# Optimization experiments

Hardware: AMD Instinct MI355X
Metric: run time of the kernel (lower is better)

## Reference

```python
import jax, jax.numpy as jnp
import numpy as np

V_IPC, N_ROLES, D = 50000, 16, 256
B, L = 2048, 64
F_BIB, H1, H2, D_OUT = 512, 1024, 1024, 512
N_EXP, N_CLS = 8, 10
LN_EPS = 1e-5


def setup_inputs() -> dict:
    key = jax.random.key(0)
    ks = jax.random.split(key, 24)
    s = 0.05
    ipc_emb = jax.random.normal(ks[0], (V_IPC, D), jnp.float32) * s
    ipc_emb = ipc_emb.at[0].set(0.0)  # padding_idx=0
    role_emb = jax.random.normal(ks[1], (N_ROLES, D), jnp.float32) * s
    role_emb = role_emb.at[0].set(0.0)
    inp = {
        "ipc_indices": jax.random.randint(ks[2], (B, L), 0, V_IPC),
        "role_indices": jax.random.randint(ks[3], (B, L), 0, N_ROLES),
        "bibliometric_features": jax.random.normal(ks[4], (B, F_BIB), jnp.float32),
        "ipc_padding_mask": jax.random.randint(ks[5], (B, L), 0, 2).astype(jnp.int32),
        "top_k": 2,
        "ipc_emb": ipc_emb,
        "role_emb": role_emb,
        "Wq": jax.random.normal(ks[6], (D, D), jnp.float32) * s,
        "bq": jnp.zeros((D,), jnp.float32),
        "Wk": jax.random.normal(ks[7], (D, D), jnp.float32) * s,
        "bk": jnp.zeros((D,), jnp.float32),
        "Wv": jax.random.normal(ks[8], (D, D), jnp.float32) * s,
        "bv": jnp.zeros((D,), jnp.float32),
        "global_context": jax.random.normal(ks[9], (D,), jnp.float32) * s,
        "ln_g": jnp.ones((D,), jnp.float32),
        "ln_b": jnp.zeros((D,), jnp.float32),
        "gate_W": jax.random.normal(ks[10], (D, N_EXP), jnp.float32) * s,
        "gate_b": jnp.zeros((N_EXP,), jnp.float32),
        "expert_biases": jnp.zeros((N_EXP,), jnp.float32),
        "W1": jax.random.normal(ks[11], (N_EXP, F_BIB, H1), jnp.float32) * s,
        "b1": jnp.zeros((N_EXP, H1), jnp.float32),
        "W2": jax.random.normal(ks[12], (N_EXP, H1, H2), jnp.float32) * s,
        "b2": jnp.zeros((N_EXP, H2), jnp.float32),
        "W3": jax.random.normal(ks[13], (N_EXP, H2, D_OUT), jnp.float32) * s,
        "b3": jnp.zeros((N_EXP, D_OUT), jnp.float32),
        "head_W": jax.random.normal(ks[14], (D_OUT, N_CLS), jnp.float32) * s,
        "head_b": jnp.zeros((N_CLS,), jnp.float32),
    }
    return inp


def reference(ipc_indices, role_indices, bibliometric_features, ipc_padding_mask, top_k,
              ipc_emb, role_emb, Wq, bq, Wk, bk, Wv, bv, global_context, ln_g, ln_b,
              gate_W, gate_b, expert_biases, W1, b1, W2, b2, W3, b3, head_W, head_b):
    # embeddings + role combine  -> [B, L, D]
    x = ipc_emb[ipc_indices] + role_emb[role_indices]
    # attention pooling with a global learned query (same query for every batch row)
    keys = x @ Wk + bk                                  # [B, L, D]
    values = x @ Wv + bv                                # [B, L, D]
    q = global_context @ Wq + bq                        # [D]
    scores = jnp.einsum('d,bld->bl', q, keys)           # [B, L]
    scores = jnp.where(ipc_padding_mask == 0, -1e9, scores)
    attn = jax.nn.softmax(scores, axis=-1)              # [B, L]
    pooled = jnp.einsum('bl,bld->bd', attn, values)     # [B, D]
    mu = pooled.mean(-1, keepdims=True)
    var = ((pooled - mu) ** 2).mean(-1, keepdims=True)
    router_in = (pooled - mu) / jnp.sqrt(var + LN_EPS) * ln_g + ln_b
    # router: select with biased scores, gate with unbiased scores
    affinity = router_in @ gate_W + gate_b              # [B, E]
    sel_scores = affinity + expert_biases
    _, idx = jax.lax.top_k(sel_scores, top_k)           # [B, K]
    gw = jax.nn.softmax(jnp.take_along_axis(affinity, idx, axis=-1), axis=-1)  # [B, K]
    # dense all-expert MLP (reference form of masked per-expert loop)
    h = jax.nn.relu(jnp.einsum('bi,eih->ebh', bibliometric_features, W1) + b1[:, None, :])
    h = jax.nn.relu(jnp.einsum('ebh,ehj->ebj', h, W2) + b2[:, None, :])
    eo = jnp.einsum('ebj,ejo->ebo', h, W3) + b3[:, None, :]  # [E, B, O]
    # gather each token's top-k expert outputs and combine
    bidx = jnp.arange(idx.shape[0])[:, None]            # [B, 1]
    sel_out = eo[idx, bidx]                             # [B, K, O]
    moe_out = jnp.einsum('bk,bko->bo', gw, sel_out)     # [B, O]
    logits = moe_out @ head_W + head_b                  # [B, n_classes]
    return logits, idx
```

## Files before the change

### kernel.cpp

```cpp
#include <hip/hip_runtime.h>
#include <hip/hip_bf16.h>
#include <math.h>


#define LN_EPS 1e-5f

typedef __bf16 bf16_t;
typedef __bf16 bf16x8 __attribute__((ext_vector_type(8)));
typedef float f32x4 __attribute__((ext_vector_type(4)));

struct f4x2 { float4 a, b; };
__device__ __forceinline__ f4x2 ldA8(const float* p) {
  f4x2 v; v.a = *(const float4*)p; v.b = *(const float4*)(p + 4); return v;
}
__device__ __forceinline__ bf16x8 cvt8(const f4x2& v) {
  bf16x8 o;
  o[0] = (bf16_t)v.a.x; o[1] = (bf16_t)v.a.y; o[2] = (bf16_t)v.a.z; o[3] = (bf16_t)v.a.w;
  o[4] = (bf16_t)v.b.x; o[5] = (bf16_t)v.b.y; o[6] = (bf16_t)v.b.z; o[7] = (bf16_t)v.b.w;
  return o;
}

__global__ __launch_bounds__(256)
void transpose_prep(const float* __restrict__ W1, const float* __restrict__ W2,
                    const float* __restrict__ W3, bf16_t* __restrict__ B1,
                    bf16_t* __restrict__ B2, bf16_t* __restrict__ B3,
                    const float* __restrict__ Wq, const float* __restrict__ bq,
                    const float* __restrict__ Wk, const float* __restrict__ bk,
                    const float* __restrict__ gc, float* __restrict__ kq_out) {
  __shared__ float tile[64][65];
  const int z = blockIdx.z;
  if (z == 24) {
    if (blockIdx.y >= 2) return;
    float* q = &tile[0][0];
    float* red = &tile[0][0] + 256;
    const int t = threadIdx.x, bi = blockIdx.y * 16 + blockIdx.x;
    float s = bq[t];
    for (int d = 0; d < 256; d++) s += gc[d] * Wq[d * 256 + t];
    q[t] = s;
    __syncthreads();
    const int rl = t >> 5, sl = t & 31;
    const int r = bi * 8 + rl;
    float p = 0.f;
#pragma unroll
    for (int i = 0; i < 8; i++) { const int d = sl + 32 * i; p += Wk[r * 256 + d] * q[d]; }
#pragma unroll
    for (int o = 16; o > 0; o >>= 1) p += __shfl_down(p, o, 32);
    if (sl == 0) kq_out[r] = p;
    if (bi == 0) {
      float z2 = q[t] * bk[t];
      const int lane = t & 63, wave = t >> 6;
#pragma unroll
      for (int o = 32; o > 0; o >>= 1) z2 += __shfl_down(z2, o);
      if (lane == 0) red[wave] = z2;
      __syncthreads();
      if (t == 0) kq_out[256] = red[0] + red[1] + red[2] + red[3];
    }
    return;
  }
  const float* W; bf16_t* Bft; int K, N, e;
  if (z < 8)       { W = W1; Bft = B1; K = 512;  N = 1024; e = z; }
  else if (z < 16) { W = W2; Bft = B2; K = 1024; N = 1024; e = z - 8; }
  else             { W = W3; Bft = B3; K = 1024; N = 512;  e = z - 16; }
  const int n0 = blockIdx.x * 64, k0 = blockIdx.y * 64;
  if (n0 >= N || k0 >= K) return;
  const float* Wp = W + (size_t)e * K * N;
  bf16_t* Bp = Bft + (size_t)e * N * K;
  const int tq = threadIdx.x & 15, th = threadIdx.x >> 4;
#pragma unroll
  for (int i = 0; i < 4; i++) {
    const int row = th + 16 * i;
    *(float4*)&tile[row][tq * 4] = *(const float4*)(Wp + (size_t)(k0 + row) * N + n0 + tq * 4);
  }
  __syncthreads();
  const int lane = threadIdx.x & 63, sub = threadIdx.x >> 6;
  const int nk = K >> 5;
#pragma unroll
  for (int it = 0; it < 2; it++) {
    const int fid = sub + it * 4;
    const int ntl = fid & 3, ktl = fid >> 2;
    const int n_l = ntl * 16 + (lane & 15);
    const int k_l = ktl * 32 + (lane >> 4) * 8;
    bf16x8 o;
#pragma unroll
    for (int j = 0; j < 8; j++) o[j] = (bf16_t)tile[k_l + j][n_l];
    const size_t idx = ((((size_t)(n0 >> 4) + ntl) * nk + (k0 >> 5) + ktl) * 64 + lane) * 8;
    *(bf16x8*)(Bp + idx) = o;
  }
}

__global__ __launch_bounds__(256)
void score_tab_kernel(const float* __restrict__ ipc_emb,
                      const float* __restrict__ role_emb,
                      const float* __restrict__ kq_qbk, float* __restrict__ tab) {
  const int wave = threadIdx.x >> 6, lane = threadIdx.x & 63;
  const float4 kq = *(const float4*)(kq_qbk + lane * 4);
  const int base = (blockIdx.x * 4 + wave) * 32;
  for (int i = 0; i < 32; i++) {
    const int r = base + i;
    if (r >= 50016) return;
    const float* src = (r < 50000) ? (ipc_emb + (size_t)r * 256)
                                   : (role_emb + (size_t)(r - 50000) * 256);
    const float4 v = *(const float4*)(src + lane * 4);
    float p = v.x * kq.x + v.y * kq.y + v.z * kq.z + v.w * kq.w;
#pragma unroll
    for (int o = 32; o > 0; o >>= 1) p += __shfl_down(p, o);
    if (lane == 0) tab[r] = (r < 50000) ? p : (p + kq_qbk[256]);
  }
}

__global__ __launch_bounds__(256)
void xbar_kernel(const int* __restrict__ ipc_idx, const int* __restrict__ role_idx,
                 const int* __restrict__ maskp,
                 const float* __restrict__ ipc_emb, const float* __restrict__ role_emb,
                 const float* __restrict__ tab, float* __restrict__ xbar_g) {
  const int b = blockIdx.x;
  __shared__ float attn_s[64];
  __shared__ __align__(16) float part[4][256];
  const int t = threadIdx.x, wave = t >> 6, lane = t & 63;
  const int d0 = lane * 4;
  if (wave == 0) {
    const int ii = ipc_idx[b * 64 + lane], ri = role_idx[b * 64 + lane];
    float s = tab[ii] + tab[50000 + ri];
    s = (maskp[b * 64 + lane] == 0) ? -1e9f : s;
    float m = s;
#pragma unroll
    for (int o = 32; o > 0; o >>= 1) m = fmaxf(m, __shfl_xor(m, o));
    const float ev = expf(s - m);
    float sum = ev;
#pragma unroll
    for (int o = 32; o > 0; o >>= 1) sum += __shfl_xor(sum, o);
    attn_s[lane] = ev / sum;
  }
  __syncthreads();
  float p0 = 0.f, p1 = 0.f, p2 = 0.f, p3 = 0.f;
  for (int l = wave; l < 64; l += 4) {
    const float a = attn_s[l];
    if (a == 0.f) continue;
    const int ii = ipc_idx[b * 64 + l], ri = role_idx[b * 64 + l];
    const float4 xe = *(const float4*)(ipc_emb + (size_t)ii * 256 + d0);
    const float4 re = *(const float4*)(role_emb + (size_t)ri * 256 + d0);
    p0 += a * (xe.x + re.x); p1 += a * (xe.y + re.y);
    p2 += a * (xe.z + re.z); p3 += a * (xe.w + re.w);
  }
  *(float4*)&part[wave][d0] = make_float4(p0, p1, p2, p3);
  __syncthreads();
  xbar_g[(size_t)b * 256 + t] = part[0][t] + part[1][t] + part[2][t] + part[3][t];
}

__global__ __launch_bounds__(256)
void pool_kernel(const float* __restrict__ xbar_g, const float* __restrict__ Wv,
                 const float* __restrict__ bvec,
                 const float* __restrict__ ln_g, const float* __restrict__ ln_b,
                 const float* __restrict__ gate_W, const float* __restrict__ gate_b,
                 const float* __restrict__ expert_biases,
                 float* __restrict__ out_idx_f, int* __restrict__ ws_idx,
                 float* __restrict__ ws_gw) {
  const int rb = blockIdx.x * 8;
  __shared__ __align__(16) float xs[8][256];
  __shared__ __align__(16) float ps[8][260];
  const int t = threadIdx.x, wave = t >> 6, lane = t & 63;
  for (int i = t; i < 512; i += 256)
    ((float4*)xs)[i] = ((const float4*)(xbar_g + (size_t)rb * 256))[i];
  __syncthreads();
  const float* x0 = xs[wave * 2];
  const float* x1 = xs[wave * 2 + 1];
  f32x4 acc0 = {0.f, 0.f, 0.f, 0.f}, acc1 = {0.f, 0.f, 0.f, 0.f};
  for (int d = 0; d < 256; d += 4) {
    const float4 xa = *(const float4*)(x0 + d);
    const float4 xb = *(const float4*)(x1 + d);
#pragma unroll
    for (int j = 0; j < 4; j++) {
      const float4 wv = *(const float4*)(Wv + (size_t)(d + j) * 256 + lane * 4);
      const float aj = (&xa.x)[j], bj = (&xb.x)[j];
      acc0.x += aj * wv.x; acc0.y += aj * wv.y; acc0.z += aj * wv.z; acc0.w += aj * wv.w;
      acc1.x += bj * wv.x; acc1.y += bj * wv.y; acc1.z += bj * wv.z; acc1.w += bj * wv.w;
    }
  }
  const float4 bvv = *(const float4*)(bvec + lane * 4);
  acc0.x += bvv.x; acc0.y += bvv.y; acc0.z += bvv.z; acc0.w += bvv.w;
  acc1.x += bvv.x; acc1.y += bvv.y; acc1.z += bvv.z; acc1.w += bvv.w;
  *(f32x4*)&ps[wave * 2][lane * 4] = acc0;
  *(f32x4*)&ps[wave * 2 + 1][lane * 4] = acc1;
  __syncthreads();
  const float4 lg = *(const float4*)(ln_g + lane * 4);
  const float4 lb = *(const float4*)(ln_b + lane * 4);
#pragma unroll
  for (int rr = 0; rr < 2; rr++) {
    const int r = wave * 2 + rr;
    const float4 v = *(const float4*)&ps[r][lane * 4];
    float s1 = v.x + v.y + v.z + v.w;
#pragma unroll
    for (int o = 32; o > 0; o >>= 1) s1 += __shfl_xor(s1, o);
    const float mu = s1 * (1.f / 256.f);
    const float4 df = make_float4(v.x - mu, v.y - mu, v.z - mu, v.w - mu);
    float s2 = df.x * df.x + df.y * df.y + df.z * df.z + df.w * df.w;
#pragma unroll
    for (int o = 32; o > 0; o >>= 1) s2 += __shfl_xor(s2, o);
    const float inv = 1.f / sqrtf(s2 * (1.f / 256.f) + LN_EPS);
    f32x4 rv;
    rv[0] = df.x * inv * lg.x + lb.x; rv[1] = df.y * inv * lg.y + lb.y;
    rv[2] = df.z * inv * lg.z + lb.z; rv[3] = df.w * inv * lg.w + lb.w;
    f32x4 pa = {0.f, 0.f, 0.f, 0.f}, pb = {0.f, 0.f, 0.f, 0.f};
#pragma unroll
    for (int k = 0; k < 4; k++) {
      const int d = lane * 4 + k;
      const f32x4 g0 = *(const f32x4*)(gate_W + d * 8);
      const f32x4 g1 = *(const f32x4*)(gate_W + d * 8 + 4);
      pa += rv[k] * g0;
      pb += rv[k] * g1;
    }
#pragma unroll
    for (int o = 32; o > 0; o >>= 1) {
      pa[0] += __shfl_down(pa[0], o); pa[1] += __shfl_down(pa[1], o);
      pa[2] += __shfl_down(pa[2], o); pa[3] += __shfl_down(pa[3], o);
      pb[0] += __shfl_down(pb[0], o); pb[1] += __shfl_down(pb[1], o);
      pb[2] += __shfl_down(pb[2], o); pb[3] += __shfl_down(pb[3], o);
    }
    if (lane == 0) {
      float aff[8];
#pragma unroll
      for (int j = 0; j < 4; j++) { aff[j] = pa[j] + gate_b[j]; aff[4 + j] = pb[j] + gate_b[4 + j]; }
      float b0 = -1e30f; int i0 = 0;
#pragma unroll
      for (int j = 0; j < 8; j++) {
        const float s = aff[j] + expert_biases[j];
        if (s > b0) { b0 = s; i0 = j; }
      }
      float b1v = -1e30f; int i1 = 0;
#pragma unroll
      for (int j = 0; j < 8; j++) {
        const float s = aff[j] + expert_biases[j];
        if (j != i0 && s > b1v) { b1v = s; i1 = j; }
      }
      const float a0 = aff[i0], a1 = aff[i1];
      const float m = fmaxf(a0, a1);
      const float e0 = expf(a0 - m), e1 = expf(a1 - m);
      const float invs = 1.f / (e0 + e1);
      const int bg = rb + r;
      ws_idx[bg * 2] = i0; ws_idx[bg * 2 + 1] = i1;
      ws_gw[bg * 2] = e0 * invs; ws_gw[bg * 2 + 1] = e1 * invs;
      out_idx_f[bg * 2] = (float)i0; out_idx_f[bg * 2 + 1] = (float)i1;
    }
  }
}

__global__ __launch_bounds__(256)
void pack_kernel(const int* __restrict__ ws_idx, int* __restrict__ list_token,
                 int* __restrict__ a_of, int* __restrict__ offsets_g) {
  __shared__ int cnt[8]; __shared__ int off[9]; __shared__ int fill[8];
  const int t = threadIdx.x;
  if (t < 8) cnt[t] = 0;
  __syncthreads();
  for (int a = t; a < 4096; a += 256) atomicAdd(&cnt[ws_idx[a]], 1);
  __syncthreads();
  if (t == 0) {
    off[0] = 0;
    for (int e = 0; e < 8; e++) off[e + 1] = off[e] + ((cnt[e] + 63) & ~63);
  }
  __syncthreads();
  if (t < 8) fill[t] = off[t];
  if (t < 9) offsets_g[t] = off[t];
  for (int a = t; a < 4608; a += 256) list_token[a] = 0;
  __syncthreads();
  for (int a = t; a < 4096; a += 256) {
    const int e = ws_idx[a];
    const int pos = atomicAdd(&fill[e], 1);
    list_token[pos] = a >> 1;
    a_of[a] = pos;
  }
}

template <int NT, bool RELU>
__global__ __launch_bounds__(256)
void expert_gemm_g1(const float* __restrict__ bib, const int* __restrict__ list_token,
                    const bf16_t* __restrict__ Bft, const float* __restrict__ bias,
                    bf16_t* __restrict__ C, const int* __restrict__ offsets) {
  constexpr int K = 512, nk = K / 32;
  const int e = blockIdx.z;
  const int seg_hi = offsets[e + 1];
  const int blk_row = offsets[e] + blockIdx.y * 128;
  if (blk_row >= seg_hi) return;
  const int wave = threadIdx.x >> 6, lane = threadIdx.x & 63;
  const int row0 = blk_row + wave * 32;
  if (row0 >= seg_hi) return;
  const int n0 = blockIdx.x * 64;
  const int tok0 = list_token[row0 + (lane & 15)];
  const int tok1 = list_token[row0 + 16 + (lane & 15)];
  const float* Ap0 = bib + (size_t)tok0 * 512 + (lane >> 4) * 8;
  const float* Ap1 = bib + (size_t)tok1 * 512 + (lane >> 4) * 8;
  const bf16_t* Bp = Bft + (size_t)e * NT * K + ((size_t)(n0 >> 4) * nk * 512 + lane * 8);
  f32x4 acc[2][4];
#pragma unroll
  for (int i = 0; i < 2; i++)
#pragma unroll
    for (int j = 0; j < 4; j++) acc[i][j] = (f32x4){0.f, 0.f, 0.f, 0.f};
  f4x2 aS[2][2]; bf16x8 bX[2][4];
  aS[0][0] = ldA8(Ap0); aS[0][1] = ldA8(Ap1);
#pragma unroll
  for (int ni = 0; ni < 4; ni++) bX[0][ni] = *(const bf16x8*)(Bp + (size_t)ni * nk * 512);
#pragma unroll
  for (int kt = 0; kt < nk; kt++) {
    const int cur = kt & 1, nxt = cur ^ 1;
    if (kt + 1 < nk) {
      aS[nxt][0] = ldA8(Ap0 + (kt + 1) * 32);
      aS[nxt][1] = ldA8(Ap1 + (kt + 1) * 32);
#pragma unroll
      for (int ni = 0; ni < 4; ni++)
        bX[nxt][ni] = *(const bf16x8*)(Bp + ((size_t)ni * nk + kt + 1) * 512);
    }
    const bf16x8 a0 = cvt8(aS[cur][0]), a1 = cvt8(aS[cur][1]);
#pragma unroll
    for (int ni = 0; ni < 4; ni++) {
      acc[0][ni] = __builtin_amdgcn_mfma_f32_16x16x32_bf16(a0, bX[cur][ni], acc[0][ni], 0, 0, 0);
      acc[1][ni] = __builtin_amdgcn_mfma_f32_16x16x32_bf16(a1, bX[cur][ni], acc[1][ni], 0, 0, 0);
    }
  }
  const int fr = lane & 15, q = lane >> 4;
#pragma unroll
  for (int ni = 0; ni < 4; ni++) {
    const int col = n0 + ni * 16 + fr;
    const float bv = bias[e * NT + col];
#pragma unroll
    for (int mi = 0; mi < 2; mi++) {
#pragma unroll
      for (int r = 0; r < 4; r++) {
        const int row = row0 + mi * 16 + q * 4 + r;
        float v = acc[mi][ni][r] + bv;
        if (RELU) v = fmaxf(v, 0.f);
        C[(size_t)row * NT + col] = (bf16_t)v;
      }
    }
  }
}

template <int K, int NT, bool RELU, typename OUT_T>
__global__ __launch_bounds__(256)
void expert_gemm_ft(const bf16_t* __restrict__ A, const bf16_t* __restrict__ Bft,
                    const float* __restrict__ bias, OUT_T* __restrict__ C,
                    const int* __restrict__ offsets) {
  constexpr int nk = K / 32;
  const int e = blockIdx.z;
  const int seg_hi = offsets[e + 1];
  const int blk_row = offsets[e] + blockIdx.y * 128;
  if (blk_row >= seg_hi) return;
  const int wave = threadIdx.x >> 6, lane = threadIdx.x & 63;
  const int row0 = blk_row + wave * 32;
  if (row0 >= seg_hi) return;
  const int n0 = blockIdx.x * 64;
  const bf16_t* Ap = A + (size_t)(row0 + (lane & 15)) * K + ((lane >> 4) * 8);
  const bf16_t* Bp = Bft + (size_t)e * NT * K + ((size_t)(n0 >> 4) * nk * 512 + lane * 8);
  f32x4 acc[2][4];
#pragma unroll
  for (int i = 0; i < 2; i++)
#pragma unroll
    for (int j = 0; j < 4; j++) acc[i][j] = (f32x4){0.f, 0.f, 0.f, 0.f};
  bf16x8 aX[2][2], bX[2][4];
#pragma unroll
  for (int mi = 0; mi < 2; mi++) aX[0][mi] = *(const bf16x8*)(Ap + mi * 16 * K);
#pragma unroll
  for (int ni = 0; ni < 4; ni++) bX[0][ni] = *(const bf16x8*)(Bp + (size_t)ni * nk * 512);
#pragma unroll
  for (int kt = 0; kt < nk; kt++) {
    const int cur = kt & 1, nxt = cur ^ 1;
    if (kt + 1 < nk) {
#pragma unroll
      for (int mi = 0; mi < 2; mi++)
        aX[nxt][mi] = *(const bf16x8*)(Ap + mi * 16 * K + (kt + 1) * 32);
#pragma unroll
      for (int ni = 0; ni < 4; ni++)
        bX[nxt][ni] = *(const bf16x8*)(Bp + ((size_t)ni * nk + kt + 1) * 512);
    }
#pragma unroll
    for (int mi = 0; mi < 2; mi++)
#pragma unroll
      for (int ni = 0; ni < 4; ni++)
        acc[mi][ni] = __builtin_amdgcn_mfma_f32_16x16x32_bf16(aX[cur][mi], bX[cur][ni], acc[mi][ni], 0, 0, 0);
  }
  const int fr = lane & 15, q = lane >> 4;
#pragma unroll
  for (int ni = 0; ni < 4; ni++) {
    const int col = n0 + ni * 16 + fr;
    const float bv = bias[e * NT + col];
#pragma unroll
    for (int mi = 0; mi < 2; mi++) {
#pragma unroll
      for (int r = 0; r < 4; r++) {
        const int row = row0 + mi * 16 + q * 4 + r;
        float v = acc[mi][ni][r] + bv;
        if (RELU) v = fmaxf(v, 0.f);
        C[(size_t)row * NT + col] = (OUT_T)v;
      }
    }
  }
}

__global__ __launch_bounds__(256)
void head_kernel(const float* __restrict__ O, const int* __restrict__ a_of,
                 const float* __restrict__ ws_gw, const float* __restrict__ head_W,
                 const float* __restrict__ head_b, float* __restrict__ out) {
  const int b = blockIdx.x, t = threadIdx.x;
  __shared__ float m[512];
  const int a0 = a_of[b * 2], a1 = a_of[b * 2 + 1];
  const float g0 = ws_gw[b * 2], g1 = ws_gw[b * 2 + 1];
  for (int d = t; d < 512; d += 256)
    m[d] = g0 * O[(size_t)a0 * 512 + d] + g1 * O[(size_t)a1 * 512 + d];
  __syncthreads();
  if (t < 160) {
    const int c = t >> 4, ch = t & 15;
    float p = 0.f;
#pragma unroll
    for (int i = 0; i < 32; i++) {
      const int d = i * 16 + ch;
      p += m[d] * head_W[d * 10 + c];
    }
#pragma unroll
    for (int o = 8; o > 0; o >>= 1) p += __shfl_down(p, o, 16);
    if (ch == 0) out[b * 10 + c] = p + head_b[c];
  }
}

extern "C" void kernel_launch(void* const* d_in, const int* in_sizes, int n_in,
                              void* d_out, int out_size, void* d_ws, size_t ws_size,
                              hipStream_t stream) {
  const int* ipc_idx = (const int*)d_in[0];
  const int* role_idx = (const int*)d_in[1];
  const float* bib = (const float*)d_in[2];
  const int* maskp = (const int*)d_in[3];
  const float* ipc_emb = (const float*)d_in[5];
  const float* role_emb = (const float*)d_in[6];
  const float* Wq = (const float*)d_in[7];
  const float* bq = (const float*)d_in[8];
  const float* Wk = (const float*)d_in[9];
  const float* bk = (const float*)d_in[10];
  const float* Wv = (const float*)d_in[11];
  const float* bv = (const float*)d_in[12];
  const float* gc = (const float*)d_in[13];
  const float* ln_g = (const float*)d_in[14];
  const float* ln_b = (const float*)d_in[15];
  const float* gate_W = (const float*)d_in[16];
  const float* gate_b = (const float*)d_in[17];
  const float* exp_b = (const float*)d_in[18];
  const float* W1 = (const float*)d_in[19];
  const float* b1 = (const float*)d_in[20];
  const float* W2 = (const float*)d_in[21];
  const float* b2 = (const float*)d_in[22];
  const float* W3 = (const float*)d_in[23];
  const float* b3 = (const float*)d_in[24];
  const float* head_W = (const float*)d_in[25];
  const float* head_b = (const float*)d_in[26];

  char* ws = (char*)d_ws;
  size_t off = 0;
  auto alloc = [&](size_t bytes) -> char* {
    char* p = ws + off;
    off += (bytes + 255) & ~(size_t)255;
    return p;
  };
  float* kq_qbk = (float*)alloc(257 * 4);
  float* tab = (float*)alloc(50016 * 4);
  float* xbar_g = (float*)alloc((size_t)2048 * 256 * 4);
  int* ws_idx = (int*)alloc(4096 * 4);
  float* ws_gw = (float*)alloc(4096 * 4);
  int* list_tok = (int*)alloc(4608 * 4);
  int* a_of = (int*)alloc(4096 * 4);
  int* offs = (int*)alloc(9 * 4);
  bf16_t* W1t = (bf16_t*)alloc((size_t)8 * 1024 * 512 * 2);
  bf16_t* W2t = (bf16_t*)alloc((size_t)8 * 1024 * 1024 * 2);
  bf16_t* W3t = (bf16_t*)alloc((size_t)8 * 512 * 1024 * 2);
  bf16_t* H1c = (bf16_t*)alloc((size_t)4608 * 1024 * 2);
  bf16_t* H2c = (bf16_t*)alloc((size_t)4608 * 1024 * 2);
  float* Oc = (float*)alloc((size_t)4608 * 512 * 4);
  (void)in_sizes; (void)n_in; (void)out_size; (void)ws_size;

  float* out_logits = (float*)d_out;
  float* out_idx = (float*)d_out + 20480;

  transpose_prep<<<dim3(16, 16, 25), 256, 0, stream>>>(W1, W2, W3, W1t, W2t, W3t,
                                                       Wq, bq, Wk, bk, gc, kq_qbk);
  score_tab_kernel<<<391, 256, 0, stream>>>(ipc_emb, role_emb, kq_qbk, tab);
  xbar_kernel<<<2048, 256, 0, stream>>>(ipc_idx, role_idx, maskp, ipc_emb, role_emb,
                                        tab, xbar_g);
  pool_kernel<<<256, 256, 0, stream>>>(xbar_g, Wv, bv, ln_g, ln_b, gate_W, gate_b,
                                       exp_b, out_idx, ws_idx, ws_gw);
  pack_kernel<<<1, 256, 0, stream>>>(ws_idx, list_tok, a_of, offs);
  expert_gemm_g1<1024, true><<<dim3(16, 36, 8), 256, 0, stream>>>(bib, list_tok, W1t, b1, H1c, offs);
  expert_gemm_ft<1024, 1024, true, bf16_t><<<dim3(16, 36, 8), 256, 0, stream>>>(H1c, W2t, b2, H2c, offs);
  expert_gemm_ft<1024, 512, false, float><<<dim3(8, 36, 8), 256, 0, stream>>>(H2c, W3t, b3, Oc, offs);
  head_kernel<<<2048, 256, 0, stream>>>(Oc, a_of, ws_gw, head_W, head_b, out_logits);
}
```

Before: 378.6 us.

## Fuse score table into xbar kernel and split pool GEMV over d

Drops the precomputed score table over the whole 50k-row vocabulary. Each xbar block now gathers its 64 embedding rows once into registers, computes the attention scores from them, and reuses the same registers for the weighted sum. This removes a full pass over the embedding table and the second gather of the same rows. The pool kernel also gives each wave a quarter of the d range for all 8 rows instead of all of d for 2 rows, then reduces the partials through LDS. The cost is higher register pressure from the 16 float4 values held per thread and a larger shared-memory buffer.

```diff
diff --git a/kernel.cpp b/kernel.cpp
--- a/kernel.cpp
+++ b/kernel.cpp
@@ -89,43 +89,52 @@
 }
 
 __global__ __launch_bounds__(256)
-void score_tab_kernel(const float* __restrict__ ipc_emb,
-                      const float* __restrict__ role_emb,
-                      const float* __restrict__ kq_qbk, float* __restrict__ tab) {
-  const int wave = threadIdx.x >> 6, lane = threadIdx.x & 63;
-  const float4 kq = *(const float4*)(kq_qbk + lane * 4);
-  const int base = (blockIdx.x * 4 + wave) * 32;
-  for (int i = 0; i < 32; i++) {
-    const int r = base + i;
-    if (r >= 50016) return;
-    const float* src = (r < 50000) ? (ipc_emb + (size_t)r * 256)
-                                   : (role_emb + (size_t)(r - 50000) * 256);
-    const float4 v = *(const float4*)(src + lane * 4);
-    float p = v.x * kq.x + v.y * kq.y + v.z * kq.z + v.w * kq.w;
-#pragma unroll
-    for (int o = 32; o > 0; o >>= 1) p += __shfl_down(p, o);
-    if (lane == 0) tab[r] = (r < 50000) ? p : (p + kq_qbk[256]);
-  }
-}
-
-__global__ __launch_bounds__(256)
 void xbar_kernel(const int* __restrict__ ipc_idx, const int* __restrict__ role_idx,
                  const int* __restrict__ maskp,
                  const float* __restrict__ ipc_emb, const float* __restrict__ role_emb,
-                 const float* __restrict__ tab, float* __restrict__ xbar_g) {
+                 const float* __restrict__ kq_qbk, float* __restrict__ xbar_g) {
   const int b = blockIdx.x;
+  __shared__ float scores_s[64];
   __shared__ float attn_s[64];
   __shared__ __align__(16) float part[4][256];
   const int t = threadIdx.x, wave = t >> 6, lane = t & 63;
-  const int d0 = lane * 4;
+  const float4 kq = *(const float4*)(kq_qbk + lane * 4);
+  const float qbk = kq_qbk[256];
+  const int rbase = b * 64 + wave * 16;
+  float4 x[16];
+  int mk[16];
+#pragma unroll
+  for (int i = 0; i < 16; i++) {
+    mk[i] = maskp[rbase + i];
+    if (mk[i] != 0) {
+      const int ii = ipc_idx[rbase + i], ri = role_idx[rbase + i];
+      const float4 xe = *(const float4*)(ipc_emb + (size_t)ii * 256 + lane * 4);
+      const float4 re = *(const float4*)(role_emb + (size_t)ri * 256 + lane * 4);
+      x[i] = make_float4(xe.x + re.x, xe.y + re.y, xe.z + re.z, xe.w + re.w);
+    } else {
+      x[i] = make_float4(0.f, 0.f, 0.f, 0.f);
+    }
+  }
+#pragma unroll
+  for (int i = 0; i < 16; i++) {
+    float s;
+    if (mk[i] != 0) {
+      s = x[i].x * kq.x + x[i].y * kq.y + x[i].z * kq.z + x[i].w * kq.w;
+#pragma unroll
+      for (int o = 32; o > 0; o >>= 1) s += __shfl_xor(s, o);
+      s += qbk;
+    } else {
+      s = -1e9f;
+    }
+    if (lane == 0) scores_s[wave * 16 + i] = s;
+  }
+  __syncthreads();
   if (wave == 0) {
-    const int ii = ipc_idx[b * 64 + lane], ri = role_idx[b * 64 + lane];
-    float s = tab[ii] + tab[50000 + ri];
-    s = (maskp[b * 64 + lane] == 0) ? -1e9f : s;
-    float m = s;
+    const float sv = scores_s[lane];
+    float m = sv;
 #pragma unroll
     for (int o = 32; o > 0; o >>= 1) m = fmaxf(m, __shfl_xor(m, o));
-    const float ev = expf(s - m);
+    const float ev = expf(sv - m);
     float sum = ev;
 #pragma unroll
     for (int o = 32; o > 0; o >>= 1) sum += __shfl_xor(sum, o);
@@ -133,16 +142,12 @@
   }
   __syncthreads();
   float p0 = 0.f, p1 = 0.f, p2 = 0.f, p3 = 0.f;
-  for (int l = wave; l < 64; l += 4) {
-    const float a = attn_s[l];
-    if (a == 0.f) continue;
-    const int ii = ipc_idx[b * 64 + l], ri = role_idx[b * 64 + l];
-    const float4 xe = *(const float4*)(ipc_emb + (size_t)ii * 256 + d0);
-    const float4 re = *(const float4*)(role_emb + (size_t)ri * 256 + d0);
-    p0 += a * (xe.x + re.x); p1 += a * (xe.y + re.y);
-    p2 += a * (xe.z + re.z); p3 += a * (xe.w + re.w);
-  }
-  *(float4*)&part[wave][d0] = make_float4(p0, p1, p2, p3);
+#pragma unroll
+  for (int i = 0; i < 16; i++) {
+    const float a = attn_s[wave * 16 + i];
+    p0 += a * x[i].x; p1 += a * x[i].y; p2 += a * x[i].z; p3 += a * x[i].w;
+  }
+  *(float4*)&part[wave][lane * 4] = make_float4(p0, p1, p2, p3);
   __syncthreads();
   xbar_g[(size_t)b * 256 + t] = part[0][t] + part[1][t] + part[2][t] + part[3][t];
 }
@@ -157,42 +162,51 @@
                  float* __restrict__ ws_gw) {
   const int rb = blockIdx.x * 8;
   __shared__ __align__(16) float xs[8][256];
-  __shared__ __align__(16) float ps[8][260];
+  __shared__ __align__(16) float pp[4][8][256];
   const int t = threadIdx.x, wave = t >> 6, lane = t & 63;
   for (int i = t; i < 512; i += 256)
     ((float4*)xs)[i] = ((const float4*)(xbar_g + (size_t)rb * 256))[i];
   __syncthreads();
-  const float* x0 = xs[wave * 2];
-  const float* x1 = xs[wave * 2 + 1];
-  f32x4 acc0 = {0.f, 0.f, 0.f, 0.f}, acc1 = {0.f, 0.f, 0.f, 0.f};
-  for (int d = 0; d < 256; d += 4) {
-    const float4 xa = *(const float4*)(x0 + d);
-    const float4 xb = *(const float4*)(x1 + d);
+  f32x4 acc[8];
+#pragma unroll
+  for (int r = 0; r < 8; r++) acc[r] = (f32x4){0.f, 0.f, 0.f, 0.f};
+  const int dbase = wave * 64;
+  for (int dd = 0; dd < 64; dd += 4) {
+    float4 xr[8];
+#pragma unroll
+    for (int r = 0; r < 8; r++) xr[r] = *(const float4*)&xs[r][dbase + dd];
 #pragma unroll
     for (int j = 0; j < 4; j++) {
-      const float4 wv = *(const float4*)(Wv + (size_t)(d + j) * 256 + lane * 4);
-      const float aj = (&xa.x)[j], bj = (&xb.x)[j];
-      acc0.x += aj * wv.x; acc0.y += aj * wv.y; acc0.z += aj * wv.z; acc0.w += aj * wv.w;
-      acc1.x += bj * wv.x; acc1.y += bj * wv.y; acc1.z += bj * wv.z; acc1.w += bj * wv.w;
-    }
-  }
+      const float4 wv = *(const float4*)(Wv + (size_t)(dbase + dd + j) * 256 + lane * 4);
+#pragma unroll
+      for (int r = 0; r < 8; r++) {
+        const float xv = (&xr[r].x)[j];
+        acc[r][0] += xv * wv.x; acc[r][1] += xv * wv.y;
+        acc[r][2] += xv * wv.z; acc[r][3] += xv * wv.w;
+      }
+    }
+  }
+#pragma unroll
+  for (int r = 0; r < 8; r++) *(f32x4*)&pp[wave][r][lane * 4] = acc[r];
+  __syncthreads();
   const float4 bvv = *(const float4*)(bvec + lane * 4);
-  acc0.x += bvv.x; acc0.y += bvv.y; acc0.z += bvv.z; acc0.w += bvv.w;
-  acc1.x += bvv.x; acc1.y += bvv.y; acc1.z += bvv.z; acc1.w += bvv.w;
-  *(f32x4*)&ps[wave * 2][lane * 4] = acc0;
-  *(f32x4*)&ps[wave * 2 + 1][lane * 4] = acc1;
-  __syncthreads();
   const float4 lg = *(const float4*)(ln_g + lane * 4);
   const float4 lb = *(const float4*)(ln_b + lane * 4);
 #pragma unroll
   for (int rr = 0; rr < 2; rr++) {
     const int r = wave * 2 + rr;
-    const float4 v = *(const float4*)&ps[r][lane * 4];
-    float s1 = v.x + v.y + v.z + v.w;
+    f32x4 v = *(const f32x4*)&pp[0][r][lane * 4];
+#pragma unroll
+    for (int w2 = 1; w2 < 4; w2++) {
+      const f32x4 qv = *(const f32x4*)&pp[w2][r][lane * 4];
+      v[0] += qv[0]; v[1] += qv[1]; v[2] += qv[2]; v[3] += qv[3];
+    }
+    v[0] += bvv.x; v[1] += bvv.y; v[2] += bvv.z; v[3] += bvv.w;
+    float s1 = v[0] + v[1] + v[2] + v[3];
 #pragma unroll
     for (int o = 32; o > 0; o >>= 1) s1 += __shfl_xor(s1, o);
     const float mu = s1 * (1.f / 256.f);
-    const float4 df = make_float4(v.x - mu, v.y - mu, v.z - mu, v.w - mu);
+    const float4 df = make_float4(v[0] - mu, v[1] - mu, v[2] - mu, v[3] - mu);
     float s2 = df.x * df.x + df.y * df.y + df.z * df.z + df.w * df.w;
 #pragma unroll
     for (int o = 32; o > 0; o >>= 1) s2 += __shfl_xor(s2, o);
@@ -457,7 +471,6 @@
     return p;
   };
   float* kq_qbk = (float*)alloc(257 * 4);
-  float* tab = (float*)alloc(50016 * 4);
   float* xbar_g = (float*)alloc((size_t)2048 * 256 * 4);
   int* ws_idx = (int*)alloc(4096 * 4);
   float* ws_gw = (float*)alloc(4096 * 4);
@@ -477,9 +490,8 @@
 
   transpose_prep<<<dim3(16, 16, 25), 256, 0, stream>>>(W1, W2, W3, W1t, W2t, W3t,
                                                        Wq, bq, Wk, bk, gc, kq_qbk);
-  score_tab_kernel<<<391, 256, 0, stream>>>(ipc_emb, role_emb, kq_qbk, tab);
   xbar_kernel<<<2048, 256, 0, stream>>>(ipc_idx, role_idx, maskp, ipc_emb, role_emb,
-                                        tab, xbar_g);
+                                        kq_qbk, xbar_g);
   pool_kernel<<<256, 256, 0, stream>>>(xbar_g, Wv, bv, ln_g, ln_b, gate_W, gate_b,
                                        exp_b, out_idx, ws_idx, ws_gw);
   pack_kernel<<<1, 256, 0, stream>>>(ws_idx, list_tok, a_of, offs);
```

After: 370.0 us. -2.3%, faster.
